# Kernel tuning notes

Measured on AMD Instinct MI355X. Metric: run time of the kernel, lower is better.

The kernel has to match this reference:

```python
import jax, jax.numpy as jnp
import numpy as np
from jax.scipy.linalg import expm

S = 2048  # state size = 2**max_num_qubits
B = 4096  # batch


def setup_inputs() -> dict:
    key = jax.random.key(0)
    k1, k2, k3 = jax.random.split(key, 3)
    inputs = jax.random.normal(k1, (B, S), dtype=jnp.float32)
    M_real = 0.1 * jax.random.normal(k2, (S, S), dtype=jnp.float32)
    M_imag = 0.1 * jax.random.normal(k3, (S, S), dtype=jnp.float32)
    bias = jnp.zeros((S,), dtype=jnp.float32)
    qubit_gate = jnp.ones((S,), dtype=jnp.float32)
    return {"inputs": inputs, "M_real": M_real, "M_imag": M_imag,
            "bias": bias, "qubit_gate": qubit_gate}


def reference(inputs, M_real, M_imag, bias, qubit_gate):
    # l2-normalize along last axis (matches tf.linalg.l2_normalize)
    norm = jnp.sqrt(jnp.maximum(jnp.sum(inputs * inputs, axis=-1, keepdims=True), 1e-12))
    norm_inputs = inputs / norm
    # skew-symmetric generators -> orthogonal-like transforms via expm
    A = M_real - M_real.T
    Bm = M_imag - M_imag.T
    U = expm(A) @ expm(Bm)
    transformed = norm_inputs @ U + bias  # [B, S]
    measured = jnp.square(transformed)
    gate_probs = jax.nn.softmax(qubit_gate)  # [S]
    gated_output = measured * gate_probs
    return gated_output, gate_probs
```

## Files before the change

### kernel.cpp

```cpp
#include <hip/hip_runtime.h>
#include <math.h>

#define SD 2048
#define BDIM 4096

typedef _Float16 f16;
using f16x8 = __attribute__((ext_vector_type(8))) f16;
using f32x4 = __attribute__((ext_vector_type(4))) float;

#define EPS_CROSS 4.8828125e-4f
#define LSCALE    2048.0f

__device__ __forceinline__ void fsplit(float x, f16& h, f16& l) {
    h = (f16)x;
    l = (f16)((x - (float)h) * LSCALE);
}
__device__ __forceinline__ float fcomb(f16 h, f16 l) {
    return (float)h + (float)l * EPS_CROSS;
}
__device__ __forceinline__ void glds16(const void* g, void* l) {
    __builtin_amdgcn_global_load_lds(
        (const __attribute__((address_space(1))) unsigned int*)g,
        (__attribute__((address_space(3))) unsigned int*)l, 16, 0, 0);
}

struct GArgs {
    const f16 *Ah, *Al, *Bh, *Bl;
    f16 *CAh, *CAl; float sA, dA;
    f16 *C2h, *C2l; float s2, d2;
    f16 *CBh, *CBl; float sB, dB;
    float *C32; const float *bias, *gate;
};

template<int OUT>
__global__ __launch_bounds__(256, 2)
void gsplit_k(GArgs gz0, GArgs gz1)
{
    const GArgs g = blockIdx.z ? gz1 : gz0;
    __shared__ char smem[65536];
    const int tid  = threadIdx.x;
    const int lane = tid & 63, wid = tid >> 6;
    const int row0 = blockIdx.y * 128, col0 = blockIdx.x * 128;

    const int lrow = lane >> 2;
    const int gsl  = (lane & 3) ^ (lrow & 3);
    const f16* splane = (wid == 0) ? g.Ah : (wid == 1) ? g.Al
                      : (wid == 2) ? g.Bh : g.Bl;
    const int  sbase  = (wid < 2) ? row0 : col0;
    const size_t sgoff = (size_t)(sbase + lrow) * SD + gsl * 8;

    auto stage = [&](int buf, int k0) {
        char* lb = smem + buf * 32768 + wid * 8192;
        const f16* gp = splane + sgoff + k0;
        #pragma unroll
        for (int s = 0; s < 8; ++s)
            glds16(gp + (size_t)s * 16 * SD, lb + s * 1024);
    };

    const int lr = lane & 15, lg = lane >> 4;
    const int wm = wid >> 1, wn = wid & 1;
    const int afo = (wm*64 + lr)*64 + ((lg ^ (lr & 3)) << 4);
    const int bfo = (wn*64 + lr)*64 + ((lg ^ (lr & 3)) << 4);

    f32x4 ch[4][4], cx[4][4];
    #pragma unroll
    for (int m = 0; m < 4; ++m)
    #pragma unroll
    for (int n = 0; n < 4; ++n) { ch[m][n] = (f32x4)0.f; cx[m][n] = (f32x4)0.f; }

    stage(0, 0);
    for (int kt = 0; kt < SD / 32; ++kt) {
        const int cur = kt & 1;
        __syncthreads();
        if (kt + 1 < SD / 32) stage(cur ^ 1, (kt + 1) * 32);
        const char* base = smem + cur * 32768;
        f16x8 ah[4], al[4], bh[4], bl[4];
        #pragma unroll
        for (int m = 0; m < 4; ++m) {
            ah[m] = *(const f16x8*)(base +     0 + afo + m*1024);
            al[m] = *(const f16x8*)(base +  8192 + afo + m*1024);
        }
        #pragma unroll
        for (int n = 0; n < 4; ++n) {
            bh[n] = *(const f16x8*)(base + 16384 + bfo + n*1024);
            bl[n] = *(const f16x8*)(base + 24576 + bfo + n*1024);
        }
        #pragma unroll
        for (int m = 0; m < 4; ++m)
        #pragma unroll
        for (int n = 0; n < 4; ++n) {
            ch[m][n] = __builtin_amdgcn_mfma_f32_16x16x32_f16(ah[m], bh[n], ch[m][n], 0, 0, 0);
            cx[m][n] = __builtin_amdgcn_mfma_f32_16x16x32_f16(ah[m], bl[n], cx[m][n], 0, 0, 0);
            cx[m][n] = __builtin_amdgcn_mfma_f32_16x16x32_f16(al[m], bh[n], cx[m][n], 0, 0, 0);
        }
    }

    const int erow = wm*64 + lg*4;
    const int ecol = wn*64 + lr;

    if (OUT == 0) {
        f16* lds16 = (f16*)smem;
        auto dumpPlane = [&](f16* dst, bool transp) {
            #pragma unroll
            for (int i = 0; i < 8; ++i) {
                int chunk = i * 256 + tid;
                int r = chunk >> 4, cs = chunk & 15;
                f16x8 v = *(const f16x8*)(lds16 + r * 136 + cs * 8);
                size_t go = transp ? ((size_t)(col0 + r) * SD + row0 + cs * 8)
                                   : ((size_t)(row0 + r) * SD + col0 + cs * 8);
                *(f16x8*)(dst + go) = v;
            }
        };
        auto writePair = [&](f16* dh, f16* dl, float s, float d, bool transp) {
            #pragma unroll
            for (int pl = 0; pl < 2; ++pl) {
                __syncthreads();
                #pragma unroll
                for (int m = 0; m < 4; ++m)
                #pragma unroll
                for (int n = 0; n < 4; ++n)
                #pragma unroll
                for (int q = 0; q < 4; ++q) {
                    int rl = erow + m*16 + q, cl = ecol + n*16;
                    float v  = ch[m][n][q] + EPS_CROSS * cx[m][n][q];
                    float vv = s * v + (((row0 + rl) == (col0 + cl)) ? d : 0.f);
                    f16 h, l; fsplit(vv, h, l);
                    int idx = transp ? (cl * 136 + rl) : (rl * 136 + cl);
                    lds16[idx] = pl ? l : h;
                }
                __syncthreads();
                dumpPlane(pl ? dl : dh, transp);
            }
        };
        if (g.CAh) writePair(g.CAh, g.CAl, g.sA, g.dA, false);
        if (g.C2h) writePair(g.C2h, g.C2l, g.s2, g.d2, false);
        if (g.CBh) writePair(g.CBh, g.CBl, g.sB, g.dB, true);
    } else {
        float* lds32 = (float*)smem;
        #pragma unroll
        for (int h = 0; h < 2; ++h) {
            __syncthreads();
            if (wn == h) {
                #pragma unroll
                for (int m = 0; m < 4; ++m)
                #pragma unroll
                for (int n = 0; n < 4; ++n) {
                    int cl = ecol + n*16;
                    float b  = g.bias[col0 + cl];
                    float ga = g.gate[col0 + cl];
                    #pragma unroll
                    for (int q = 0; q < 4; ++q) {
                        int rl = erow + m*16 + q;
                        float v = ch[m][n][q] + EPS_CROSS * cx[m][n][q];
                        float t = v + b;
                        lds32[rl*68 + (cl - h*64)] = t * t * ga;
                    }
                }
            }
            __syncthreads();
            #pragma unroll
            for (int i = 0; i < 8; ++i) {
                int chunk = i * 256 + tid;
                int r = chunk >> 4, cs = chunk & 15;
                float4 v = *(const float4*)(lds32 + r*68 + cs*4);
                *(float4*)(g.C32 + (size_t)(row0 + r) * SD + col0 + h*64 + cs*4) = v;
            }
        }
    }
}

struct SArgs { const float* M; f16 *XAh, *XAl, *XBh, *XBl; };

__global__ __launch_bounds__(256)
void skew_split_k(SArgs sz0, SArgs sz1, float scale)
{
    const SArgs s = blockIdx.z ? sz1 : sz0;
    __shared__ float t1[32][33], t2[32][33];
    const int bx = blockIdx.x*32, by = blockIdx.y*32;
    const int tx = threadIdx.x, ty = threadIdx.y;
    #pragma unroll
    for (int r = 0; r < 32; r += 8) {
        t1[ty+r][tx] = s.M[(size_t)(by+ty+r)*SD + bx+tx];
        t2[ty+r][tx] = s.M[(size_t)(bx+ty+r)*SD + by+tx];
    }
    __syncthreads();
    #pragma unroll
    for (int r = 0; r < 32; r += 8) {
        float xs = (t1[ty+r][tx] - t2[tx][ty+r]) * scale;
        size_t idx = (size_t)(by+ty+r)*SD + bx+tx;
        f16 h, l;
        fsplit(xs, h, l);  s.XAh[idx] = h; s.XAl[idx] = l;
        fsplit(-xs, h, l); s.XBh[idx] = h; s.XBl[idx] = l;
    }
}

struct EArgs { const float* M; float cA; f16 *Ahp, *Alp; float cB; f16 *Bhp, *Blp; };

__global__ __launch_bounds__(256)
void eadd_k(EArgs ez0, EArgs ez1, float scale)
{
    const EArgs e = blockIdx.z ? ez1 : ez0;
    __shared__ float t1[32][33], t2[32][33];
    const int bx = blockIdx.x*32, by = blockIdx.y*32;
    const int tx = threadIdx.x, ty = threadIdx.y;
    #pragma unroll
    for (int r = 0; r < 32; r += 8) {
        t1[ty+r][tx] = e.M[(size_t)(by+ty+r)*SD + bx+tx];
        t2[ty+r][tx] = e.M[(size_t)(bx+ty+r)*SD + by+tx];
    }
    __syncthreads();
    #pragma unroll
    for (int r = 0; r < 32; r += 8) {
        float xs = (t1[ty+r][tx] - t2[tx][ty+r]) * scale;
        size_t idx = (size_t)(by+ty+r)*SD + bx+tx;
        f16 h, l;
        float va = fcomb(e.Ahp[idx], e.Alp[idx]) + e.cA * xs;
        fsplit(va, h, l); e.Ahp[idx] = h; e.Alp[idx] = l;
        if (e.Bhp) {
            float vb = fcomb(e.Bhp[idx], e.Blp[idx]) + e.cB * xs;
            fsplit(vb, h, l); e.Bhp[idx] = h; e.Blp[idx] = l;
        }
    }
}

__global__ __launch_bounds__(256)
void rownorm_k(const float* __restrict__ in, float* __restrict__ rn)
{
    const int row = blockIdx.x;
    const float4* p = (const float4*)(in + (size_t)row * SD);
    float ss = 0.f;
    for (int i = threadIdx.x; i < SD / 4; i += 256) {
        float4 v = p[i];
        ss += v.x*v.x + v.y*v.y + v.z*v.z + v.w*v.w;
    }
#pragma unroll
    for (int o = 32; o; o >>= 1) ss += __shfl_down(ss, o);
    __shared__ float part[4];
    if ((threadIdx.x & 63) == 0) part[threadIdx.x >> 6] = ss;
    __syncthreads();
    if (threadIdx.x == 0) {
        const float t = part[0] + part[1] + part[2] + part[3];
        rn[row] = 1.0f / sqrtf(fmaxf(t, 1e-12f));
    }
}

__global__ __launch_bounds__(256)
void nsplit_k(const float* __restrict__ in, const float* __restrict__ rn,
              f16* __restrict__ ph, f16* __restrict__ pl)
{
    const size_t gid  = (size_t)blockIdx.x * 256 + threadIdx.x;
    const size_t base = gid * 8;
    const float r = rn[(int)(base >> 11)];
    float4 a = *(const float4*)(in + base);
    float4 b = *(const float4*)(in + base + 4);
    float v[8] = {a.x, a.y, a.z, a.w, b.x, b.y, b.z, b.w};
    f16x8 h, l;
    #pragma unroll
    for (int j = 0; j < 8; ++j) {
        f16 hh, ll; fsplit(v[j] * r, hh, ll);
        h[j] = hh; l[j] = ll;
    }
    *(f16x8*)(ph + base) = h;
    *(f16x8*)(pl + base) = l;
}

__global__ __launch_bounds__(256)
void softmax_k(const float* __restrict__ q, float* __restrict__ pws,
               float* __restrict__ pout)
{
    __shared__ float red[4];
    const int tid = threadIdx.x;
    float m = -INFINITY;
    for (int i = tid; i < SD; i += 256) m = fmaxf(m, q[i]);
#pragma unroll
    for (int o = 32; o; o >>= 1) m = fmaxf(m, __shfl_down(m, o));
    if ((tid & 63) == 0) red[tid >> 6] = m;
    __syncthreads();
    const float gm = fmaxf(fmaxf(red[0], red[1]), fmaxf(red[2], red[3]));
    float s = 0.f;
    for (int i = tid; i < SD; i += 256) s += expf(q[i] - gm);
#pragma unroll
    for (int o = 32; o; o >>= 1) s += __shfl_down(s, o);
    __syncthreads();
    if ((tid & 63) == 0) red[tid >> 6] = s;
    __syncthreads();
    const float inv = 1.0f / (red[0] + red[1] + red[2] + red[3]);
    for (int i = tid; i < SD; i += 256) {
        const float val = expf(q[i] - gm) * inv;
        pws[i] = val;
        pout[i] = val;
    }
}

struct Pair { f16* h; f16* l; };

static GArgs mkG(Pair A, Pair B, Pair CA, float sA, float dA,
                 Pair C2, float s2, float d2, Pair CB, float sB, float dB)
{
    GArgs g{};
    g.Ah = A.h; g.Al = A.l; g.Bh = B.h; g.Bl = B.l;
    g.CAh = CA.h; g.CAl = CA.l; g.sA = sA; g.dA = dA;
    g.C2h = C2.h; g.C2l = C2.l; g.s2 = s2; g.d2 = d2;
    g.CBh = CB.h; g.CBl = CB.l; g.sB = sB; g.dB = dB;
    g.C32 = nullptr; g.bias = nullptr; g.gate = nullptr;
    return g;
}

struct ChainBuf { Pair p[4]; const float* Msrc; bool finalB; };

#define SC (1.0f / 16.0f)

static void expm_sched(hipStream_t st, int nz, const ChainBuf& c0, const ChainBuf& c1)
{
    const float k2 = 0.5f, k3 = 1.f/6.f, k4 = 1.f/24.f, k5 = 1.f/120.f, k6 = 1.f/720.f;
    const Pair NP{nullptr, nullptr};
    const dim3 tb(256);
    const dim3 gsq(SD/128, SD/128, nz);
    const dim3 gtr(SD/32, SD/32, nz), ttr(32, 8);

    auto G = [&](GArgs a, GArgs b) { gsplit_k<0><<<gsq, tb, 0, st>>>(a, b); };
    auto E = [&](EArgs a, EArgs b) { eadd_k<<<gtr, ttr, 0, st>>>(a, b, SC); };

    SArgs s0{c0.Msrc, c0.p[0].h, c0.p[0].l, c0.p[1].h, c0.p[1].l};
    SArgs s1{c1.Msrc, c1.p[0].h, c1.p[0].l, c1.p[1].h, c1.p[1].l};
    skew_split_k<<<gtr, ttr, 0, st>>>(s0, s1, SC);

    auto g1 = [&](const ChainBuf& c) {
        return mkG(c.p[0], c.p[1], c.p[2], k6, k4, c.p[3], 1.f, 0.f, NP, 0.f, 0.f); };
    G(g1(c0), g1(c1));
    auto e1 = [&](const ChainBuf& c) {
        return EArgs{c.Msrc, k5, c.p[2].h, c.p[2].l, 0.f, nullptr, nullptr}; };
    E(e1(c0), e1(c1));
    auto g2 = [&](const ChainBuf& c) {
        return mkG(c.p[2], c.p[3], c.p[0], 1.f, k2, NP, 0.f, 0.f, NP, 0.f, 0.f); };
    G(g2(c0), g2(c1));
    auto e2 = [&](const ChainBuf& c) {
        return EArgs{c.Msrc, k3, c.p[0].h, c.p[0].l, 0.f, nullptr, nullptr}; };
    E(e2(c0), e2(c1));
    auto g3 = [&](const ChainBuf& c) {
        return mkG(c.p[0], c.p[3], c.p[1], 1.f, 1.f, NP, 0.f, 0.f, c.p[2], 1.f, 1.f); };
    G(g3(c0), g3(c1));
    auto e3 = [&](const ChainBuf& c) {
        return EArgs{c.Msrc, 1.f, c.p[1].h, c.p[1].l, -1.f, c.p[2].h, c.p[2].l}; };
    E(e3(c0), e3(c1));

    auto sqF = [&](const ChainBuf& c, int ia, int ib, int oa, int ob) {
        return mkG(c.p[ia], c.p[ib], c.p[oa], 1.f, 0.f, NP, 0.f, 0.f, c.p[ob], 1.f, 0.f); };
    G(sqF(c0, 1, 2, 0, 3), sqF(c1, 1, 2, 0, 3));
    G(sqF(c0, 0, 3, 1, 2), sqF(c1, 0, 3, 1, 2));
    G(sqF(c0, 1, 2, 0, 3), sqF(c1, 1, 2, 0, 3));
    auto sqL = [&](const ChainBuf& c) {
        Pair ca = c.finalB ? NP : c.p[1];
        Pair cb = c.finalB ? c.p[1] : NP;
        return mkG(c.p[0], c.p[3], ca, 1.f, 0.f, NP, 0.f, 0.f, cb, 1.f, 0.f); };
    G(sqL(c0), sqL(c1));
}

extern "C" void kernel_launch(void* const* d_in, const int* in_sizes, int n_in,
                              void* d_out, int out_size, void* d_ws, size_t ws_size,
                              hipStream_t stream)
{
    const float* inputs = (const float*)d_in[0];
    const float* Mr     = (const float*)d_in[1];
    const float* Mi     = (const float*)d_in[2];
    const float* bias   = (const float*)d_in[3];
    const float* qg     = (const float*)d_in[4];
    float* out = (float*)d_out;

    const size_t PLANE = (size_t)SD * SD * sizeof(f16);
    const size_t PAIRB = 2 * PLANE;
    char* wsb = (char*)d_ws;
    char* ob  = (char*)d_out;

    auto WP = [&](int i) { char* b = wsb + (size_t)i * PAIRB;
                           return Pair{(f16*)b, (f16*)(b + PLANE)}; };
    auto DP = [&](int i) { char* b = ob + (size_t)i * PAIRB;
                           return Pair{(f16*)b, (f16*)(b + PLANE)}; };

    const bool fused = ws_size >= 6 * PAIRB + 64 * 1024;
    const size_t smallOff = (fused ? 6 : 3) * PAIRB;
    float* rnorm = (float*)(wsb + smallOff);
    float* gatew = rnorm + 4096;
    float* gout  = out + (size_t)BDIM * SD;

    const dim3 tb(256);
    const dim3 gsq1(SD/128, SD/128, 1);
    const dim3 gbt(SD/128, BDIM/128, 1);

    rownorm_k<<<BDIM, tb, 0, stream>>>(inputs, rnorm);
    softmax_k<<<1, tb, 0, stream>>>(qg, gatew, gout);

    Pair EA, EB, UF;
    int ninSlotA, ninSlotB;
    if (fused) {
        ChainBuf c0{{WP(0), WP(1), WP(2), WP(3)}, Mr, false};
        ChainBuf c1{{WP(4), WP(5), DP(0), DP(1)}, Mi, true};
        expm_sched(stream, 2, c0, c1);
        EA = WP(1); EB = WP(5); UF = WP(0);
        ninSlotA = 2; ninSlotB = 3;
    } else {
        ChainBuf c0{{WP(0), WP(1), DP(0), DP(1)}, Mr, false};
        expm_sched(stream, 1, c0, c0);
        ChainBuf c1{{WP(0), WP(2), DP(0), DP(1)}, Mi, true};
        expm_sched(stream, 1, c1, c1);
        EA = WP(1); EB = WP(2); UF = WP(0);
        ninSlotA = 1; ninSlotB = 2;
    }

    {
        GArgs u = mkG(EA, EB, Pair{nullptr,nullptr}, 0.f, 0.f,
                      Pair{nullptr,nullptr}, 0.f, 0.f, UF, 1.f, 0.f);
        gsplit_k<0><<<gsq1, tb, 0, stream>>>(u, u);
    }
    f16* ninh = (f16*)(wsb + (size_t)ninSlotA * PAIRB);
    f16* ninl = (f16*)(wsb + (size_t)ninSlotB * PAIRB);
    nsplit_k<<<(BDIM * SD / 8) / 256, tb, 0, stream>>>(inputs, rnorm, ninh, ninl);
    {
        GArgs b{};
        b.Ah = ninh; b.Al = ninl;
        b.Bh = UF.h; b.Bl = UF.l;
        b.C32 = out; b.bias = bias; b.gate = gatew;
        gsplit_k<2><<<gbt, tb, 0, stream>>>(b, b);
    }

    (void)in_sizes; (void)n_in; (void)out_size;
}
```

Measured before the change: 1.180 ms.

## Restructure split-f16 GEMM into 256x128 tiles with triple-buffered interleaved staging

The split-precision GEMM kernel moves to 512-thread blocks computing 256x128 tiles. It uses a three-stage LDS ring held in dynamic shared memory, and issues global-to-LDS loads between the MFMA groups so data movement overlaps compute. It adds wave priority hints, a remapping of block IDs across XCDs, a new LDS swizzle, and wider epilogue stores for both plain and transposed outputs. The large dynamic LDS footprint allows only one block per CU, and the kernel depends on the runtime accepting a launch with more than 64KB of dynamic LDS.

```diff
diff --git a/kernel.cpp b/kernel.cpp
--- a/kernel.cpp
+++ b/kernel.cpp
@@ -10,6 +10,9 @@
 
 #define EPS_CROSS 4.8828125e-4f
 #define LSCALE    2048.0f
+
+#define BUFB   49152
+#define SMEMB  147456
 
 __device__ __forceinline__ void fsplit(float x, f16& h, f16& l) {
     h = (f16)x;
@@ -33,34 +36,41 @@
 };
 
 template<int OUT>
-__global__ __launch_bounds__(256, 2)
+__global__ __launch_bounds__(512, 2)
 void gsplit_k(GArgs gz0, GArgs gz1)
 {
     const GArgs g = blockIdx.z ? gz1 : gz0;
-    __shared__ char smem[65536];
-    const int tid  = threadIdx.x;
+    extern __shared__ char smem[];
+    const int tid = threadIdx.x;
     const int lane = tid & 63, wid = tid >> 6;
-    const int row0 = blockIdx.y * 128, col0 = blockIdx.x * 128;
-
-    const int lrow = lane >> 2;
-    const int gsl  = (lane & 3) ^ (lrow & 3);
-    const f16* splane = (wid == 0) ? g.Ah : (wid == 1) ? g.Al
-                      : (wid == 2) ? g.Bh : g.Bl;
-    const int  sbase  = (wid < 2) ? row0 : col0;
-    const size_t sgoff = (size_t)(sbase + lrow) * SD + gsl * 8;
-
-    auto stage = [&](int buf, int k0) {
-        char* lb = smem + buf * 32768 + wid * 8192;
-        const f16* gp = splane + sgoff + k0;
-        #pragma unroll
-        for (int s = 0; s < 8; ++s)
-            glds16(gp + (size_t)s * 16 * SD, lb + s * 1024);
+
+    const int gx = gridDim.x, nwg = gx * gridDim.y;
+    int id = blockIdx.x + gx * blockIdx.y;
+    id = (id & 7) * (nwg >> 3) + (id >> 3);
+    const int bx = id % gx, by = id / gx;
+    const int row0 = by * 256, col0 = bx * 128;
+
+    const int kslot = (tid & 3) ^ ((tid >> 3) & 3);
+    const int srow  = tid >> 2;
+    const size_t asrc = (size_t)(row0 + srow) * SD + kslot * 8;
+    const size_t bsrc = (size_t)(col0 + srow) * SD + kslot * 8;
+
+    auto stA = [&](int buf, int k0, const f16* pl, int lofs) {
+        char* lb = smem + buf * BUFB + lofs + wid * 1024;
+        const f16* gp = pl + asrc + k0;
+        glds16(gp, lb);
+        glds16(gp + (size_t)128 * SD, lb + 8192);
+    };
+    auto stB = [&](int buf, int k0, const f16* pl, int lofs) {
+        char* lb = smem + buf * BUFB + lofs + wid * 1024;
+        glds16(pl + bsrc + k0, lb);
     };
 
     const int lr = lane & 15, lg = lane >> 4;
     const int wm = wid >> 1, wn = wid & 1;
-    const int afo = (wm*64 + lr)*64 + ((lg ^ (lr & 3)) << 4);
-    const int bfo = (wn*64 + lr)*64 + ((lg ^ (lr & 3)) << 4);
+    const int sxo = (lg ^ ((lr >> 1) & 3)) << 4;
+    const int aro = (wm * 64 + lr) * 64 + sxo;
+    const int bro = (wn * 64 + lr) * 64 + sxo;
 
     f32x4 ch[4][4], cx[4][4];
     #pragma unroll
@@ -68,68 +78,99 @@
     #pragma unroll
     for (int n = 0; n < 4; ++n) { ch[m][n] = (f32x4)0.f; cx[m][n] = (f32x4)0.f; }
 
-    stage(0, 0);
-    for (int kt = 0; kt < SD / 32; ++kt) {
-        const int cur = kt & 1;
-        __syncthreads();
-        if (kt + 1 < SD / 32) stage(cur ^ 1, (kt + 1) * 32);
-        const char* base = smem + cur * 32768;
-        f16x8 ah[4], al[4], bh[4], bl[4];
+    stA(0, 0, g.Ah, 0);     stA(0, 0, g.Al, 16384);
+    stB(0, 0, g.Bh, 32768); stB(0, 0, g.Bl, 40960);
+    stA(1, 32, g.Ah, 0);     stA(1, 32, g.Al, 16384);
+    stB(1, 32, g.Bh, 32768); stB(1, 32, g.Bl, 40960);
+    asm volatile("s_waitcnt vmcnt(6)" ::: "memory");
+    __builtin_amdgcn_s_barrier();
+    asm volatile("" ::: "memory");
+
+    f16x8 bhf[4], blf[4];
+
+    for (int kt = 0; kt < 64; ++kt) {
+        const char* bb = smem + (kt % 3) * BUFB;
+        const int  nb  = (kt + 2) % 3;
+        const int  nk0 = (kt + 2) * 32;
+        const bool st  = (kt + 2) < 64;
         #pragma unroll
-        for (int m = 0; m < 4; ++m) {
-            ah[m] = *(const f16x8*)(base +     0 + afo + m*1024);
-            al[m] = *(const f16x8*)(base +  8192 + afo + m*1024);
+        for (int p = 0; p < 4; ++p) {
+            if (p == 0) {
+                #pragma unroll
+                for (int nt = 0; nt < 4; ++nt) {
+                    bhf[nt] = *(const f16x8*)(bb + 32768 + bro + nt * 1024);
+                    blf[nt] = *(const f16x8*)(bb + 40960 + bro + nt * 1024);
+                }
+            }
+            f16x8 ah = *(const f16x8*)(bb +     0 + aro + p * 1024);
+            f16x8 al = *(const f16x8*)(bb + 16384 + aro + p * 1024);
+            if (st) {
+                if (p == 0) stA(nb, nk0, g.Ah, 0);
+                if (p == 1) stA(nb, nk0, g.Al, 16384);
+                if (p == 2) { stB(nb, nk0, g.Bh, 32768); stB(nb, nk0, g.Bl, 40960); }
+            }
+            __builtin_amdgcn_s_barrier();
+            asm volatile("s_waitcnt lgkmcnt(0)" ::: "memory");
+            __builtin_amdgcn_s_setprio(1);
+            #pragma unroll
+            for (int nt = 0; nt < 4; ++nt)
+                ch[p][nt] = __builtin_amdgcn_mfma_f32_16x16x32_f16(ah, bhf[nt], ch[p][nt], 0, 0, 0);
+            #pragma unroll
+            for (int nt = 0; nt < 4; ++nt)
+                cx[p][nt] = __builtin_amdgcn_mfma_f32_16x16x32_f16(ah, blf[nt], cx[p][nt], 0, 0, 0);
+            #pragma unroll
+            for (int nt = 0; nt < 4; ++nt)
+                cx[p][nt] = __builtin_amdgcn_mfma_f32_16x16x32_f16(al, bhf[nt], cx[p][nt], 0, 0, 0);
+            __builtin_amdgcn_s_setprio(0);
+            if (p == 3) {
+                if (kt < 62)       asm volatile("s_waitcnt vmcnt(6)" ::: "memory");
+                else if (kt == 62) asm volatile("s_waitcnt vmcnt(0)" ::: "memory");
+            }
+            __builtin_amdgcn_s_barrier();
+            asm volatile("" ::: "memory");
         }
-        #pragma unroll
-        for (int n = 0; n < 4; ++n) {
-            bh[n] = *(const f16x8*)(base + 16384 + bfo + n*1024);
-            bl[n] = *(const f16x8*)(base + 24576 + bfo + n*1024);
-        }
-        #pragma unroll
-        for (int m = 0; m < 4; ++m)
-        #pragma unroll
-        for (int n = 0; n < 4; ++n) {
-            ch[m][n] = __builtin_amdgcn_mfma_f32_16x16x32_f16(ah[m], bh[n], ch[m][n], 0, 0, 0);
-            cx[m][n] = __builtin_amdgcn_mfma_f32_16x16x32_f16(ah[m], bl[n], cx[m][n], 0, 0, 0);
-            cx[m][n] = __builtin_amdgcn_mfma_f32_16x16x32_f16(al[m], bh[n], cx[m][n], 0, 0, 0);
-        }
-    }
-
-    const int erow = wm*64 + lg*4;
-    const int ecol = wn*64 + lr;
+    }
+
+    const int erow = wm * 64 + lg * 4;
+    const int ecol = wn * 64 + lr;
 
     if (OUT == 0) {
         f16* lds16 = (f16*)smem;
-        auto dumpPlane = [&](f16* dst, bool transp) {
-            #pragma unroll
-            for (int i = 0; i < 8; ++i) {
-                int chunk = i * 256 + tid;
-                int r = chunk >> 4, cs = chunk & 15;
-                f16x8 v = *(const f16x8*)(lds16 + r * 136 + cs * 8);
-                size_t go = transp ? ((size_t)(col0 + r) * SD + row0 + cs * 8)
-                                   : ((size_t)(row0 + r) * SD + col0 + cs * 8);
-                *(f16x8*)(dst + go) = v;
-            }
-        };
         auto writePair = [&](f16* dh, f16* dl, float s, float d, bool transp) {
             #pragma unroll
             for (int pl = 0; pl < 2; ++pl) {
                 __syncthreads();
                 #pragma unroll
-                for (int m = 0; m < 4; ++m)
+                for (int mt = 0; mt < 4; ++mt)
                 #pragma unroll
-                for (int n = 0; n < 4; ++n)
+                for (int nt = 0; nt < 4; ++nt)
                 #pragma unroll
                 for (int q = 0; q < 4; ++q) {
-                    int rl = erow + m*16 + q, cl = ecol + n*16;
-                    float v  = ch[m][n][q] + EPS_CROSS * cx[m][n][q];
+                    int rl = erow + mt * 16 + q, cl = ecol + nt * 16;
+                    float v  = ch[mt][nt][q] + EPS_CROSS * cx[mt][nt][q];
                     float vv = s * v + (((row0 + rl) == (col0 + cl)) ? d : 0.f);
                     f16 h, l; fsplit(vv, h, l);
-                    int idx = transp ? (cl * 136 + rl) : (rl * 136 + cl);
-                    lds16[idx] = pl ? l : h;
+                    lds16[transp ? (cl * 264 + rl) : (rl * 136 + cl)] = pl ? l : h;
                 }
                 __syncthreads();
-                dumpPlane(pl ? dl : dh, transp);
+                f16* dst = pl ? dl : dh;
+                if (!transp) {
+                    #pragma unroll
+                    for (int i = 0; i < 8; ++i) {
+                        int c = i * 512 + tid;
+                        int r = c >> 4, cs = c & 15;
+                        f16x8 v = *(const f16x8*)(lds16 + r * 136 + cs * 8);
+                        *(f16x8*)(dst + (size_t)(row0 + r) * SD + col0 + cs * 8) = v;
+                    }
+                } else {
+                    #pragma unroll
+                    for (int i = 0; i < 8; ++i) {
+                        int c = i * 512 + tid;
+                        int r = c >> 5, cs = c & 31;
+                        f16x8 v = *(const f16x8*)(lds16 + r * 264 + cs * 8);
+                        *(f16x8*)(dst + (size_t)(col0 + r) * SD + row0 + cs * 8) = v;
+                    }
+                }
             }
         };
         if (g.CAh) writePair(g.CAh, g.CAl, g.sA, g.dA, false);
@@ -137,34 +178,29 @@
         if (g.CBh) writePair(g.CBh, g.CBl, g.sB, g.dB, true);
     } else {
         float* lds32 = (float*)smem;
+        __syncthreads();
         #pragma unroll
-        for (int h = 0; h < 2; ++h) {
-            __syncthreads();
-            if (wn == h) {
-                #pragma unroll
-                for (int m = 0; m < 4; ++m)
-                #pragma unroll
-                for (int n = 0; n < 4; ++n) {
-                    int cl = ecol + n*16;
-                    float b  = g.bias[col0 + cl];
-                    float ga = g.gate[col0 + cl];
-                    #pragma unroll
-                    for (int q = 0; q < 4; ++q) {
-                        int rl = erow + m*16 + q;
-                        float v = ch[m][n][q] + EPS_CROSS * cx[m][n][q];
-                        float t = v + b;
-                        lds32[rl*68 + (cl - h*64)] = t * t * ga;
-                    }
-                }
+        for (int mt = 0; mt < 4; ++mt)
+        #pragma unroll
+        for (int nt = 0; nt < 4; ++nt) {
+            int cl = ecol + nt * 16;
+            float b  = g.bias[col0 + cl];
+            float ga = g.gate[col0 + cl];
+            #pragma unroll
+            for (int q = 0; q < 4; ++q) {
+                int rl = erow + mt * 16 + q;
+                float v = ch[mt][nt][q] + EPS_CROSS * cx[mt][nt][q];
+                float t = v + b;
+                lds32[rl * 132 + cl] = t * t * ga;
             }
-            __syncthreads();
-            #pragma unroll
-            for (int i = 0; i < 8; ++i) {
-                int chunk = i * 256 + tid;
-                int r = chunk >> 4, cs = chunk & 15;
-                float4 v = *(const float4*)(lds32 + r*68 + cs*4);
-                *(float4*)(g.C32 + (size_t)(row0 + r) * SD + col0 + h*64 + cs*4) = v;
-            }
+        }
+        __syncthreads();
+        #pragma unroll
+        for (int i = 0; i < 16; ++i) {
+            int c = i * 512 + tid;
+            int r = c >> 5, cs = c & 31;
+            float4 v = *(const float4*)(lds32 + r * 132 + cs * 4);
+            *(float4*)(g.C32 + (size_t)(row0 + r) * SD + col0 + cs * 4) = v;
         }
     }
 }
@@ -314,11 +350,11 @@
 {
     const float k2 = 0.5f, k3 = 1.f/6.f, k4 = 1.f/24.f, k5 = 1.f/120.f, k6 = 1.f/720.f;
     const Pair NP{nullptr, nullptr};
-    const dim3 tb(256);
-    const dim3 gsq(SD/128, SD/128, nz);
+    const dim3 tb(512);
+    const dim3 gsq(SD/128, SD/256, nz);
     const dim3 gtr(SD/32, SD/32, nz), ttr(32, 8);
 
-    auto G = [&](GArgs a, GArgs b) { gsplit_k<0><<<gsq, tb, 0, st>>>(a, b); };
+    auto G = [&](GArgs a, GArgs b) { gsplit_k<0><<<gsq, tb, SMEMB, st>>>(a, b); };
     auto E = [&](EArgs a, EArgs b) { eadd_k<<<gtr, ttr, 0, st>>>(a, b, SC); };
 
     SArgs s0{c0.Msrc, c0.p[0].h, c0.p[0].l, c0.p[1].h, c0.p[1].l};
@@ -383,12 +419,12 @@
     float* gatew = rnorm + 4096;
     float* gout  = out + (size_t)BDIM * SD;
 
-    const dim3 tb(256);
-    const dim3 gsq1(SD/128, SD/128, 1);
-    const dim3 gbt(SD/128, BDIM/128, 1);
-
-    rownorm_k<<<BDIM, tb, 0, stream>>>(inputs, rnorm);
-    softmax_k<<<1, tb, 0, stream>>>(qg, gatew, gout);
+    const dim3 tb256(256), tb512(512);
+    const dim3 gsq1(SD/128, SD/256, 1);
+    const dim3 gbt(SD/128, BDIM/256, 1);
+
+    rownorm_k<<<BDIM, tb256, 0, stream>>>(inputs, rnorm);
+    softmax_k<<<1, tb256, 0, stream>>>(qg, gatew, gout);
 
     Pair EA, EB, UF;
     int ninSlotA, ninSlotB;
@@ -410,17 +446,17 @@
     {
         GArgs u = mkG(EA, EB, Pair{nullptr,nullptr}, 0.f, 0.f,
                       Pair{nullptr,nullptr}, 0.f, 0.f, UF, 1.f, 0.f);
-        gsplit_k<0><<<gsq1, tb, 0, stream>>>(u, u);
+        gsplit_k<0><<<gsq1, tb512, SMEMB, stream>>>(u, u);
     }
     f16* ninh = (f16*)(wsb + (size_t)ninSlotA * PAIRB);
     f16* ninl = (f16*)(wsb + (size_t)ninSlotB * PAIRB);
-    nsplit_k<<<(BDIM * SD / 8) / 256, tb, 0, stream>>>(inputs, rnorm, ninh, ninl);
+    nsplit_k<<<(BDIM * SD / 8) / 256, tb256, 0, stream>>>(inputs, rnorm, ninh, ninl);
     {
         GArgs b{};
         b.Ah = ninh; b.Al = ninl;
         b.Bh = UF.h; b.Bl = UF.l;
         b.C32 = out; b.bias = bias; b.gate = gatew;
-        gsplit_k<2><<<gbt, tb, 0, stream>>>(b, b);
+        gsplit_k<2><<<gbt, tb512, SMEMB, stream>>>(b, b);
     }
 
     (void)in_sizes; (void)n_in; (void)out_size;
```

New measurement: 1.192 ms. Within noise of the previous version (+1.0%).

## Switch split-f16 GEMM to 32x32 MFMA with XCD-aware tile remap and deeper prefetch

Applied to the files above, without the earlier changes.

Rewrites the main split-precision GEMM kernel's inner loop to use 32x32x16 MFMA instructions with a new LDS layout that drops the XOR swizzle. It issues two stages ahead with explicit vmcnt waits, a single barrier per k-step, and raises wave priority around the MFMA block. Workgroup IDs are remapped in groups of eight so neighbouring tiles land on the same XCD for L2 reuse. The aim is fewer LDS reads per MFMA and better overlap of global-to-LDS loads with compute. The risks are LDS bank conflicts from the unswizzled layout and a barrier placed after compute that may reduce overlap.

```diff
diff --git a/kernel.cpp b/kernel.cpp
--- a/kernel.cpp
+++ b/kernel.cpp
@@ -5,8 +5,8 @@
 #define BDIM 4096
 
 typedef _Float16 f16;
-using f16x8 = __attribute__((ext_vector_type(8))) f16;
-using f32x4 = __attribute__((ext_vector_type(4))) float;
+using f16x8  = __attribute__((ext_vector_type(8))) f16;
+using f32x16 = __attribute__((ext_vector_type(16))) float;
 
 #define EPS_CROSS 4.8828125e-4f
 #define LSCALE    2048.0f
@@ -38,98 +38,108 @@
 {
     const GArgs g = blockIdx.z ? gz1 : gz0;
     __shared__ char smem[65536];
-    const int tid  = threadIdx.x;
-    const int lane = tid & 63, wid = tid >> 6;
-    const int row0 = blockIdx.y * 128, col0 = blockIdx.x * 128;
-
-    const int lrow = lane >> 2;
-    const int gsl  = (lane & 3) ^ (lrow & 3);
+    const int tid = threadIdx.x, lane = tid & 63, wid = tid >> 6;
+
+    const int gx = gridDim.x, nwg = gx * gridDim.y;
+    int id = blockIdx.x + gx * blockIdx.y;
+    id = (id & 7) * (nwg >> 3) + (id >> 3);
+    const int bx = id % gx, by = id / gx;
+    const int row0 = by * 128, col0 = bx * 128;
+
     const f16* splane = (wid == 0) ? g.Ah : (wid == 1) ? g.Al
                       : (wid == 2) ? g.Bh : g.Bl;
-    const int  sbase  = (wid < 2) ? row0 : col0;
-    const size_t sgoff = (size_t)(sbase + lrow) * SD + gsl * 8;
+    const int sbase = (wid < 2) ? row0 : col0;
+    const size_t srow_off = (size_t)(sbase + lane) * SD;
+    char* const lds_plane = smem + wid * 8192;
 
     auto stage = [&](int buf, int k0) {
-        char* lb = smem + buf * 32768 + wid * 8192;
-        const f16* gp = splane + sgoff + k0;
         #pragma unroll
-        for (int s = 0; s < 8; ++s)
-            glds16(gp + (size_t)s * 16 * SD, lb + s * 1024);
+        for (int c = 0; c < 8; ++c)
+            glds16(splane + srow_off + (size_t)(c & 1) * 64 * SD + k0 + (c >> 1) * 8,
+                   lds_plane + buf * 32768 + c * 1024);
     };
 
-    const int lr = lane & 15, lg = lane >> 4;
     const int wm = wid >> 1, wn = wid & 1;
-    const int afo = (wm*64 + lr)*64 + ((lg ^ (lr & 3)) << 4);
-    const int bfo = (wn*64 + lr)*64 + ((lg ^ (lr & 3)) << 4);
-
-    f32x4 ch[4][4], cx[4][4];
-    #pragma unroll
-    for (int m = 0; m < 4; ++m)
-    #pragma unroll
-    for (int n = 0; n < 4; ++n) { ch[m][n] = (f32x4)0.f; cx[m][n] = (f32x4)0.f; }
+    const int l5 = lane >> 5, l31 = lane & 31;
+    const int aoff = l5 * 2048 + (wm * 64 + l31) * 16;
+    const int boff = 16384 + l5 * 2048 + (wn * 64 + l31) * 16;
+
+    f32x16 ch[2][2], cx[2][2];
+    #pragma unroll
+    for (int m = 0; m < 2; ++m)
+    #pragma unroll
+    for (int n = 0; n < 2; ++n) { ch[m][n] = (f32x16)0.f; cx[m][n] = (f32x16)0.f; }
 
     stage(0, 0);
-    for (int kt = 0; kt < SD / 32; ++kt) {
-        const int cur = kt & 1;
-        __syncthreads();
-        if (kt + 1 < SD / 32) stage(cur ^ 1, (kt + 1) * 32);
-        const char* base = smem + cur * 32768;
-        f16x8 ah[4], al[4], bh[4], bl[4];
+    stage(1, 32);
+    asm volatile("s_waitcnt vmcnt(8)" ::: "memory");
+    __builtin_amdgcn_s_barrier();
+
+    for (int kt = 0; kt < 64; ++kt) {
+        const char* bb = smem + (kt & 1) * 32768;
         #pragma unroll
-        for (int m = 0; m < 4; ++m) {
-            ah[m] = *(const f16x8*)(base +     0 + afo + m*1024);
-            al[m] = *(const f16x8*)(base +  8192 + afo + m*1024);
+        for (int ks = 0; ks < 2; ++ks) {
+            f16x8 a0h = *(const f16x8*)(bb + aoff + ks*4096 + 0*512);
+            f16x8 a1h = *(const f16x8*)(bb + aoff + ks*4096 + 1*512);
+            f16x8 a0l = *(const f16x8*)(bb + 8192 + aoff + ks*4096 + 0*512);
+            f16x8 a1l = *(const f16x8*)(bb + 8192 + aoff + ks*4096 + 1*512);
+            f16x8 b0h = *(const f16x8*)(bb + boff + ks*4096 + 0*512);
+            f16x8 b1h = *(const f16x8*)(bb + boff + ks*4096 + 1*512);
+            f16x8 b0l = *(const f16x8*)(bb + 8192 + boff + ks*4096 + 0*512);
+            f16x8 b1l = *(const f16x8*)(bb + 8192 + boff + ks*4096 + 1*512);
+            __builtin_amdgcn_s_setprio(1);
+            ch[0][0] = __builtin_amdgcn_mfma_f32_32x32x16_f16(a0h, b0h, ch[0][0], 0, 0, 0);
+            ch[0][1] = __builtin_amdgcn_mfma_f32_32x32x16_f16(a0h, b1h, ch[0][1], 0, 0, 0);
+            ch[1][0] = __builtin_amdgcn_mfma_f32_32x32x16_f16(a1h, b0h, ch[1][0], 0, 0, 0);
+            ch[1][1] = __builtin_amdgcn_mfma_f32_32x32x16_f16(a1h, b1h, ch[1][1], 0, 0, 0);
+            cx[0][0] = __builtin_amdgcn_mfma_f32_32x32x16_f16(a0h, b0l, cx[0][0], 0, 0, 0);
+            cx[0][1] = __builtin_amdgcn_mfma_f32_32x32x16_f16(a0h, b1l, cx[0][1], 0, 0, 0);
+            cx[1][0] = __builtin_amdgcn_mfma_f32_32x32x16_f16(a1h, b0l, cx[1][0], 0, 0, 0);
+            cx[1][1] = __builtin_amdgcn_mfma_f32_32x32x16_f16(a1h, b1l, cx[1][1], 0, 0, 0);
+            cx[0][0] = __builtin_amdgcn_mfma_f32_32x32x16_f16(a0l, b0h, cx[0][0], 0, 0, 0);
+            cx[0][1] = __builtin_amdgcn_mfma_f32_32x32x16_f16(a0l, b1h, cx[0][1], 0, 0, 0);
+            cx[1][0] = __builtin_amdgcn_mfma_f32_32x32x16_f16(a1l, b0h, cx[1][0], 0, 0, 0);
+            cx[1][1] = __builtin_amdgcn_mfma_f32_32x32x16_f16(a1l, b1h, cx[1][1], 0, 0, 0);
+            __builtin_amdgcn_s_setprio(0);
         }
-        #pragma unroll
-        for (int n = 0; n < 4; ++n) {
-            bh[n] = *(const f16x8*)(base + 16384 + bfo + n*1024);
-            bl[n] = *(const f16x8*)(base + 24576 + bfo + n*1024);
-        }
-        #pragma unroll
-        for (int m = 0; m < 4; ++m)
-        #pragma unroll
-        for (int n = 0; n < 4; ++n) {
-            ch[m][n] = __builtin_amdgcn_mfma_f32_16x16x32_f16(ah[m], bh[n], ch[m][n], 0, 0, 0);
-            cx[m][n] = __builtin_amdgcn_mfma_f32_16x16x32_f16(ah[m], bl[n], cx[m][n], 0, 0, 0);
-            cx[m][n] = __builtin_amdgcn_mfma_f32_16x16x32_f16(al[m], bh[n], cx[m][n], 0, 0, 0);
-        }
-    }
-
-    const int erow = wm*64 + lg*4;
-    const int ecol = wn*64 + lr;
+        asm volatile("s_waitcnt vmcnt(0)" ::: "memory");
+        __builtin_amdgcn_s_barrier();
+        if (kt + 2 < 64) stage(kt & 1, (kt + 2) * 32);
+    }
+
+    const int orow = wm * 64 + 4 * l5;
+    const int ocol = wn * 64 + l31;
 
     if (OUT == 0) {
         f16* lds16 = (f16*)smem;
-        auto dumpPlane = [&](f16* dst, bool transp) {
-            #pragma unroll
-            for (int i = 0; i < 8; ++i) {
-                int chunk = i * 256 + tid;
-                int r = chunk >> 4, cs = chunk & 15;
-                f16x8 v = *(const f16x8*)(lds16 + r * 136 + cs * 8);
-                size_t go = transp ? ((size_t)(col0 + r) * SD + row0 + cs * 8)
-                                   : ((size_t)(row0 + r) * SD + col0 + cs * 8);
-                *(f16x8*)(dst + go) = v;
-            }
-        };
         auto writePair = [&](f16* dh, f16* dl, float s, float d, bool transp) {
             #pragma unroll
             for (int pl = 0; pl < 2; ++pl) {
                 __syncthreads();
                 #pragma unroll
-                for (int m = 0; m < 4; ++m)
-                #pragma unroll
-                for (int n = 0; n < 4; ++n)
-                #pragma unroll
-                for (int q = 0; q < 4; ++q) {
-                    int rl = erow + m*16 + q, cl = ecol + n*16;
-                    float v  = ch[m][n][q] + EPS_CROSS * cx[m][n][q];
+                for (int mt = 0; mt < 2; ++mt)
+                #pragma unroll
+                for (int nt = 0; nt < 2; ++nt)
+                #pragma unroll
+                for (int r = 0; r < 16; ++r) {
+                    const int rl = orow + mt * 32 + (r & 3) + 8 * (r >> 2);
+                    const int cl = ocol + nt * 32;
+                    float v  = ch[mt][nt][r] + EPS_CROSS * cx[mt][nt][r];
                     float vv = s * v + (((row0 + rl) == (col0 + cl)) ? d : 0.f);
                     f16 h, l; fsplit(vv, h, l);
-                    int idx = transp ? (cl * 136 + rl) : (rl * 136 + cl);
-                    lds16[idx] = pl ? l : h;
+                    lds16[transp ? (cl * 136 + rl) : (rl * 136 + cl)] = pl ? l : h;
                 }
                 __syncthreads();
-                dumpPlane(pl ? dl : dh, transp);
+                f16* dst = pl ? dl : dh;
+                #pragma unroll
+                for (int i = 0; i < 8; ++i) {
+                    int c = i * 256 + tid;
+                    int rr = c >> 4, cs = c & 15;
+                    f16x8 v = *(const f16x8*)(lds16 + rr * 136 + cs * 8);
+                    size_t go = transp ? ((size_t)(col0 + rr) * SD + row0 + cs * 8)
+                                       : ((size_t)(row0 + rr) * SD + col0 + cs * 8);
+                    *(f16x8*)(dst + go) = v;
+                }
             }
         };
         if (g.CAh) writePair(g.CAh, g.CAl, g.sA, g.dA, false);
@@ -142,28 +152,28 @@
             __syncthreads();
             if (wn == h) {
                 #pragma unroll
-                for (int m = 0; m < 4; ++m)
-                #pragma unroll
-                for (int n = 0; n < 4; ++n) {
-                    int cl = ecol + n*16;
-                    float b  = g.bias[col0 + cl];
-                    float ga = g.gate[col0 + cl];
+                for (int mt = 0; mt < 2; ++mt)
+                #pragma unroll
+                for (int nt = 0; nt < 2; ++nt) {
+                    const int cl = ocol + nt * 32;
+                    const float b  = g.bias[col0 + cl];
+                    const float ga = g.gate[col0 + cl];
                     #pragma unroll
-                    for (int q = 0; q < 4; ++q) {
-                        int rl = erow + m*16 + q;
-                        float v = ch[m][n][q] + EPS_CROSS * cx[m][n][q];
+                    for (int r = 0; r < 16; ++r) {
+                        const int rl = orow + mt * 32 + (r & 3) + 8 * (r >> 2);
+                        float v = ch[mt][nt][r] + EPS_CROSS * cx[mt][nt][r];
                         float t = v + b;
-                        lds32[rl*68 + (cl - h*64)] = t * t * ga;
+                        lds32[rl * 68 + (cl - h * 64)] = t * t * ga;
                     }
                 }
             }
             __syncthreads();
             #pragma unroll
             for (int i = 0; i < 8; ++i) {
-                int chunk = i * 256 + tid;
-                int r = chunk >> 4, cs = chunk & 15;
-                float4 v = *(const float4*)(lds32 + r*68 + cs*4);
-                *(float4*)(g.C32 + (size_t)(row0 + r) * SD + col0 + h*64 + cs*4) = v;
+                int c = i * 256 + tid;
+                int rr = c >> 4, cs = c & 15;
+                float4 v = *(const float4*)(lds32 + rr * 68 + cs * 4);
+                *(float4*)(g.C32 + (size_t)(row0 + rr) * SD + col0 + h * 64 + cs * 4) = v;
             }
         }
     }
@@ -383,12 +393,12 @@
     float* gatew = rnorm + 4096;
     float* gout  = out + (size_t)BDIM * SD;
 
-    const dim3 tb(256);
+    const dim3 tb256(256);
     const dim3 gsq1(SD/128, SD/128, 1);
     const dim3 gbt(SD/128, BDIM/128, 1);
 
-    rownorm_k<<<BDIM, tb, 0, stream>>>(inputs, rnorm);
-    softmax_k<<<1, tb, 0, stream>>>(qg, gatew, gout);
+    rownorm_k<<<BDIM, tb256, 0, stream>>>(inputs, rnorm);
+    softmax_k<<<1, tb256, 0, stream>>>(qg, gatew, gout);
 
     Pair EA, EB, UF;
     int ninSlotA, ninSlotB;
@@ -410,17 +420,17 @@
     {
         GArgs u = mkG(EA, EB, Pair{nullptr,nullptr}, 0.f, 0.f,
                       Pair{nullptr,nullptr}, 0.f, 0.f, UF, 1.f, 0.f);
-        gsplit_k<0><<<gsq1, tb, 0, stream>>>(u, u);
+        gsplit_k<0><<<gsq1, tb256, 0, stream>>>(u, u);
     }
     f16* ninh = (f16*)(wsb + (size_t)ninSlotA * PAIRB);
     f16* ninl = (f16*)(wsb + (size_t)ninSlotB * PAIRB);
-    nsplit_k<<<(BDIM * SD / 8) / 256, tb, 0, stream>>>(inputs, rnorm, ninh, ninl);
+    nsplit_k<<<(BDIM * SD / 8) / 256, tb256, 0, stream>>>(inputs, rnorm, ninh, ninl);
     {
         GArgs b{};
         b.Ah = ninh; b.Al = ninl;
         b.Bh = UF.h; b.Bl = UF.l;
         b.C32 = out; b.bias = bias; b.gate = gatew;
-        gsplit_k<2><<<gbt, tb, 0, stream>>>(b, b);
+        gsplit_k<2><<<gbt, tb256, 0, stream>>>(b, b);
     }
 
     (void)in_sizes; (void)n_in; (void)out_size;
```

Measured after the change: 2.541 ms. 2.15x slower.
